# Performance work log

Hardware: AMD Instinct MI355X
Metric: run time of the kernel (lower is better)

The kernel has to match this reference:

```python
import jax, jax.numpy as jnp
import numpy as np
import itertools

DIMS = (128, 128, 128)
CHANNELS = 8
BATCH = 2_097_152


def setup_inputs() -> dict:
    key = jax.random.key(0)
    k1, k2 = jax.random.split(key)
    unList = jax.random.uniform(k1, (BATCH, len(DIMS)), dtype=jnp.float32)
    table = jax.random.uniform(k2, DIMS + (CHANNELS,), dtype=jnp.float32)  # initScale=1, initMode='R'
    return {"unList": unList, "table": table}


def reference(unList, table):
    # N-D multilinear (bilinear/trilinear) interpolated table lookup.
    dims = table.shape[:-1]
    n = len(dims)
    c = table.shape[-1]
    dims_f = jnp.asarray(dims, jnp.float32)
    # map normalized coords [0,1] onto grid [0, dim-1]
    scaled = jnp.clip(unList, 0.0, 1.0) * (dims_f - 1.0)          # [B, n]
    i0 = jnp.clip(jnp.floor(scaled), 0.0, dims_f - 2.0).astype(jnp.int32)  # lower corner
    frac = scaled - i0.astype(jnp.float32)                        # [B, n] in [0,1]
    # flatten grid for single-axis gathers
    strides = jnp.asarray([int(np.prod(dims[k + 1:])) for k in range(n)], jnp.int32)
    table_flat = table.reshape(-1, c)                             # [prod(dims), C]
    out = jnp.zeros((unList.shape[0], c), table.dtype)
    # loop over the 2^n corners (8 for 3D) -- small static loop
    for corner in itertools.product((0, 1), repeat=n):
        bits = jnp.asarray(corner, jnp.int32)                     # [n]
        flat_idx = ((i0 + bits) * strides).sum(-1)                # [B]
        w = jnp.prod(jnp.where(jnp.asarray(corner, bool), frac, 1.0 - frac), axis=-1)  # [B]
        out = out + w[:, None] * table_flat[flat_idx]             # gather + weighted sum
    return out
```

## Files before the change

### kernel.cpp

```cpp
#include <hip/hip_runtime.h>


#define DIM 128
#define CH 8
#define BINS 128
#define CHUNK 4096
#define PPT 16
#define REC_OFF 4096

__device__ __forceinline__ int key_of(float ux) {
    float sx = fminf(fmaxf(ux, 0.0f), 1.0f) * 127.0f;
    float fx0 = fminf(floorf(sx), 126.0f);
    return (int)fx0;
}

__global__ __launch_bounds__(256) void k_hist(const float* __restrict__ un,
                                              unsigned* __restrict__ hist, int batch) {
    __shared__ unsigned lh[BINS];
    for (int i = threadIdx.x; i < BINS; i += blockDim.x) lh[i] = 0;
    __syncthreads();
    int stride = gridDim.x * blockDim.x;
    for (int i = blockIdx.x * blockDim.x + threadIdx.x; i < batch; i += stride)
        atomicAdd(&lh[key_of(un[3 * i])], 1u);
    __syncthreads();
    for (int i = threadIdx.x; i < BINS; i += blockDim.x)
        if (lh[i]) atomicAdd(&hist[i], lh[i]);
}

__global__ void k_scan(const unsigned* __restrict__ hist,
                       unsigned* __restrict__ base, unsigned* __restrict__ cursor) {
    __shared__ unsigned lh[BINS];
    __shared__ unsigned lb[BINS];
    int t = threadIdx.x;
    if (t < BINS) lh[t] = hist[t];
    __syncthreads();
    if (t == 0) {
        unsigned acc = 0;
        for (int i = 0; i < BINS; ++i) { lb[i] = acc; acc += lh[i]; }
    }
    __syncthreads();
    if (t < BINS) { base[t] = lb[t]; cursor[t] = lb[t]; }
}

__global__ __launch_bounds__(256) void k_scatter(const float* __restrict__ un,
                                                 unsigned* __restrict__ cursor,
                                                 float4* __restrict__ rec, int batch) {
    __shared__ unsigned lh[BINS];
    __shared__ unsigned lbase[BINS];
    int t = threadIdx.x;
    for (int i = t; i < BINS; i += blockDim.x) lh[i] = 0;
    __syncthreads();
    int start = blockIdx.x * CHUNK;
    unsigned kr[PPT];
#pragma unroll
    for (int j = 0; j < PPT; ++j) {
        int i = start + j * 256 + t;
        if (i < batch) {
            int k = key_of(un[3 * i]);
            unsigned r = atomicAdd(&lh[k], 1u);
            kr[j] = (unsigned)k | (r << 8);
        } else kr[j] = 0xFFFFFFFFu;
    }
    __syncthreads();
    for (int i = t; i < BINS; i += blockDim.x)
        lbase[i] = lh[i] ? atomicAdd(&cursor[i], lh[i]) : 0u;
    __syncthreads();
#pragma unroll
    for (int j = 0; j < PPT; ++j) {
        int i = start + j * 256 + t;
        if (i < batch) {
            unsigned k = kr[j] & 0xFFu, r = kr[j] >> 8;
            float ux = un[3 * i], uy = un[3 * i + 1], uz = un[3 * i + 2];
            rec[lbase[k] + r] = make_float4(ux, uy, uz, __uint_as_float((unsigned)i));
        }
    }
}

__global__ __launch_bounds__(256) void k_main(const float4* __restrict__ rec,
                                              const float* __restrict__ table,
                                              float* __restrict__ out, int batch) {
    int per = gridDim.x >> 3;
    int pb = blockIdx.x;
    int lb = (pb & 7) * per + (pb >> 3);

    int t = (int)threadIdx.x;
    int lane = t & 63;
    int wave = t >> 6;
    int p = lane >> 2;
    int q = lane & 3;

    int i = lb * 64 + wave * 16 + p;
    if (i >= batch) return;

    float4 r = rec[i];
    unsigned orig = __float_as_uint(r.w);

    const float dmax = 127.0f, imax = 126.0f;
    float sx = fminf(fmaxf(r.x, 0.0f), 1.0f) * dmax;
    float sy = fminf(fmaxf(r.y, 0.0f), 1.0f) * dmax;
    float sz = fminf(fmaxf(r.z, 0.0f), 1.0f) * dmax;
    float fx0 = fminf(fmaxf(floorf(sx), 0.0f), imax);
    float fy0 = fminf(fmaxf(floorf(sy), 0.0f), imax);
    float fz0 = fminf(fmaxf(floorf(sz), 0.0f), imax);
    int x0 = (int)fx0, y0 = (int)fy0, z0 = (int)fz0;
    float fx = sx - fx0, fy = sy - fy0, fz = sz - fz0;

    float wx[2] = {1.0f - fx, fx};
    float wy[2] = {1.0f - fy, fy};
    float wzq = (q & 2) ? fz : (1.0f - fz);

    float4 acc = make_float4(0.f, 0.f, 0.f, 0.f);
#pragma unroll
    for (int bx = 0; bx < 2; ++bx) {
#pragma unroll
        for (int by = 0; by < 2; ++by) {
            const float* pbase = table +
                ((size_t)((x0 + bx) * DIM + (y0 + by)) * DIM + z0) * CH + (q << 2);
            float w = wx[bx] * wy[by] * wzq;
            float4 v = *reinterpret_cast<const float4*>(pbase);
            acc.x += w * v.x;
            acc.y += w * v.y;
            acc.z += w * v.z;
            acc.w += w * v.w;
        }
    }

    acc.x += __shfl_xor(acc.x, 2);
    acc.y += __shfl_xor(acc.y, 2);
    acc.z += __shfl_xor(acc.z, 2);
    acc.w += __shfl_xor(acc.w, 2);

    if (q < 2) {
        *reinterpret_cast<float4*>(out + (size_t)orig * CH + (q << 2)) = acc;
    }
}

__global__ __launch_bounds__(256) void k_naive(const float* __restrict__ un,
                                               const float* __restrict__ table,
                                               float* __restrict__ out, int batch) {
    int b = blockIdx.x * blockDim.x + threadIdx.x;
    if (b >= batch) return;
    float ux = un[3 * b], uy = un[3 * b + 1], uz = un[3 * b + 2];
    const float dmax = 127.0f, imax = 126.0f;
    float sx = fminf(fmaxf(ux, 0.0f), 1.0f) * dmax;
    float sy = fminf(fmaxf(uy, 0.0f), 1.0f) * dmax;
    float sz = fminf(fmaxf(uz, 0.0f), 1.0f) * dmax;
    float fx0 = fminf(fmaxf(floorf(sx), 0.0f), imax);
    float fy0 = fminf(fmaxf(floorf(sy), 0.0f), imax);
    float fz0 = fminf(fmaxf(floorf(sz), 0.0f), imax);
    int x0 = (int)fx0, y0 = (int)fy0, z0 = (int)fz0;
    float fx = sx - fx0, fy = sy - fy0, fz = sz - fz0;
    float wx[2] = {1.0f - fx, fx};
    float wy[2] = {1.0f - fy, fy};
    float wz0 = 1.0f - fz, wz1 = fz;
    float acc[CH];
#pragma unroll
    for (int c = 0; c < CH; ++c) acc[c] = 0.0f;
#pragma unroll
    for (int bx = 0; bx < 2; ++bx)
#pragma unroll
        for (int by = 0; by < 2; ++by) {
            const float* p = table + ((size_t)((x0 + bx) * DIM + (y0 + by)) * DIM + z0) * CH;
            float wxy = wx[bx] * wy[by];
            float w0 = wxy * wz0, w1 = wxy * wz1;
            float4 a0 = *reinterpret_cast<const float4*>(p + 0);
            float4 a1 = *reinterpret_cast<const float4*>(p + 4);
            float4 b0 = *reinterpret_cast<const float4*>(p + 8);
            float4 b1 = *reinterpret_cast<const float4*>(p + 12);
            acc[0] += w0 * a0.x + w1 * b0.x;  acc[1] += w0 * a0.y + w1 * b0.y;
            acc[2] += w0 * a0.z + w1 * b0.z;  acc[3] += w0 * a0.w + w1 * b0.w;
            acc[4] += w0 * a1.x + w1 * b1.x;  acc[5] += w0 * a1.y + w1 * b1.y;
            acc[6] += w0 * a1.z + w1 * b1.z;  acc[7] += w0 * a1.w + w1 * b1.w;
        }
    float4* o = reinterpret_cast<float4*>(out + (size_t)b * CH);
    o[0] = make_float4(acc[0], acc[1], acc[2], acc[3]);
    o[1] = make_float4(acc[4], acc[5], acc[6], acc[7]);
}

extern "C" void kernel_launch(void* const* d_in, const int* in_sizes, int n_in,
                              void* d_out, int out_size, void* d_ws, size_t ws_size,
                              hipStream_t stream) {
    const float* un    = (const float*)d_in[0];
    const float* table = (const float*)d_in[1];
    float* out         = (float*)d_out;
    int batch = in_sizes[0] / 3;

    size_t need = (size_t)REC_OFF + (size_t)batch * 16;
    if (ws_size < need) {
        int grid = (batch + 255) / 256;
        k_naive<<<grid, 256, 0, stream>>>(un, table, out, batch);
        return;
    }

    unsigned* hist   = (unsigned*)d_ws;
    unsigned* base   = (unsigned*)((char*)d_ws + 512);
    unsigned* cursor = (unsigned*)((char*)d_ws + 1024);
    float4*   rec    = (float4*)((char*)d_ws + REC_OFF);

    hipMemsetAsync(d_ws, 0, 1536, stream);
    k_hist<<<512, 256, 0, stream>>>(un, hist, batch);
    k_scan<<<1, 128, 0, stream>>>(hist, base, cursor);
    int nscat = (batch + CHUNK - 1) / CHUNK;
    k_scatter<<<nscat, 256, 0, stream>>>(un, cursor, rec, batch);
    int nmain = (batch + 63) / 64;
    nmain = ((nmain + 7) / 8) * 8;
    k_main<<<nmain, 256, 0, stream>>>(rec, table, out, batch);
}
```

Measured before the change: 113.3 us.

## Make gather kernel persistent with 4-point batched loads per wave

Replaces the one-point-per-16-lanes grid of 32768 blocks with a fixed grid of 2048 blocks. Each wave now walks a contiguous range of sorted records, handling 4 points per iteration and issuing all 16 table float4 loads before combining them, which raises memory-level parallelism. Address math moves to 32-bit byte offsets and a redundant clamp is dropped. The intent is to cut block launch overhead and hide gather latency, at the cost of more registers per thread (launch_bounds 256,4) and a possible tail imbalance between waves.

After: 128.4 us. +13.3%, slower.

```diff
diff --git a/kernel.cpp b/kernel.cpp
--- a/kernel.cpp
+++ b/kernel.cpp
@@ -7,6 +7,7 @@
 #define CHUNK 4096
 #define PPT 16
 #define REC_OFF 4096
+#define NMAIN 2048
 
 __device__ __forceinline__ int key_of(float ux) {
     float sx = fminf(fmaxf(ux, 0.0f), 1.0f) * 127.0f;
@@ -76,62 +77,125 @@
     }
 }
 
-__global__ __launch_bounds__(256) void k_main(const float4* __restrict__ rec,
-                                              const float* __restrict__ table,
-                                              float* __restrict__ out, int batch) {
+__global__ __launch_bounds__(256, 4) void k_main(const float4* __restrict__ rec,
+                                                 const float* __restrict__ table,
+                                                 float* __restrict__ out, int batch) {
     int per = gridDim.x >> 3;
     int pb = blockIdx.x;
     int lb = (pb & 7) * per + (pb >> 3);
 
     int t = (int)threadIdx.x;
-    int lane = t & 63;
-    int wave = t >> 6;
-    int p = lane >> 2;
-    int q = lane & 3;
-
-    int i = lb * 64 + wave * 16 + p;
-    if (i >= batch) return;
-
-    float4 r = rec[i];
-    unsigned orig = __float_as_uint(r.w);
+    int lane = t & 63, wave = t >> 6;
+    int p = lane >> 2, q = lane & 3;
+
+    int nw = (int)gridDim.x * 4;
+    int g = lb * 4 + wave;
+    long ppw = ((((long)batch + (long)nw * 64 - 1) / ((long)nw * 64)) * 64);
+    long beg = (long)g * ppw;
+    long end = beg + ppw;
+    if (end > (long)batch) end = (long)batch;
+    if (beg >= end) return;
 
     const float dmax = 127.0f, imax = 126.0f;
-    float sx = fminf(fmaxf(r.x, 0.0f), 1.0f) * dmax;
-    float sy = fminf(fmaxf(r.y, 0.0f), 1.0f) * dmax;
-    float sz = fminf(fmaxf(r.z, 0.0f), 1.0f) * dmax;
-    float fx0 = fminf(fmaxf(floorf(sx), 0.0f), imax);
-    float fy0 = fminf(fmaxf(floorf(sy), 0.0f), imax);
-    float fz0 = fminf(fmaxf(floorf(sz), 0.0f), imax);
-    int x0 = (int)fx0, y0 = (int)fy0, z0 = (int)fz0;
-    float fx = sx - fx0, fy = sy - fy0, fz = sz - fz0;
-
-    float wx[2] = {1.0f - fx, fx};
-    float wy[2] = {1.0f - fy, fy};
-    float wzq = (q & 2) ? fz : (1.0f - fz);
-
-    float4 acc = make_float4(0.f, 0.f, 0.f, 0.f);
-#pragma unroll
-    for (int bx = 0; bx < 2; ++bx) {
-#pragma unroll
-        for (int by = 0; by < 2; ++by) {
-            const float* pbase = table +
-                ((size_t)((x0 + bx) * DIM + (y0 + by)) * DIM + z0) * CH + (q << 2);
-            float w = wx[bx] * wy[by] * wzq;
-            float4 v = *reinterpret_cast<const float4*>(pbase);
-            acc.x += w * v.x;
-            acc.y += w * v.y;
-            acc.z += w * v.z;
-            acc.w += w * v.w;
-        }
-    }
-
-    acc.x += __shfl_xor(acc.x, 2);
-    acc.y += __shfl_xor(acc.y, 2);
-    acc.z += __shfl_xor(acc.z, 2);
-    acc.w += __shfl_xor(acc.w, 2);
-
-    if (q < 2) {
-        *reinterpret_cast<float4*>(out + (size_t)orig * CH + (q << 2)) = acc;
+    const char* tb = (const char*)table;
+    const unsigned qoff = (unsigned)(q << 4);
+
+    long base = beg;
+    for (; base + 64 <= end; base += 64) {
+        float4 r0 = rec[base + 0  + p];
+        float4 r1 = rec[base + 16 + p];
+        float4 r2 = rec[base + 32 + p];
+        float4 r3 = rec[base + 48 + p];
+
+        unsigned o_[4]; unsigned off_[4]; float w_[4][4];
+#define PREP(s, rr) { \
+        float sx = fminf(fmaxf(rr.x, 0.0f), 1.0f) * dmax; \
+        float sy = fminf(fmaxf(rr.y, 0.0f), 1.0f) * dmax; \
+        float sz = fminf(fmaxf(rr.z, 0.0f), 1.0f) * dmax; \
+        float fx0 = fminf(floorf(sx), imax); \
+        float fy0 = fminf(floorf(sy), imax); \
+        float fz0 = fminf(floorf(sz), imax); \
+        int x0 = (int)fx0, y0 = (int)fy0, z0 = (int)fz0; \
+        float fx = sx - fx0, fy = sy - fy0, fz = sz - fz0; \
+        float wzq = (q & 2) ? fz : (1.0f - fz); \
+        float gx = 1.0f - fx, gy = 1.0f - fy; \
+        w_[s][0] = gx * gy * wzq; \
+        w_[s][1] = gx * fy * wzq; \
+        w_[s][2] = fx * gy * wzq; \
+        w_[s][3] = fx * fy * wzq; \
+        off_[s] = (unsigned)(((x0 * 128 + y0) * 128 + z0) * 32) + qoff; \
+        o_[s] = __float_as_uint(rr.w); }
+        PREP(0, r0) PREP(1, r1) PREP(2, r2) PREP(3, r3)
+#undef PREP
+
+        float4 v00 = *(const float4*)(tb + off_[0]);
+        float4 v01 = *(const float4*)(tb + off_[0] + 4096u);
+        float4 v02 = *(const float4*)(tb + off_[0] + 524288u);
+        float4 v03 = *(const float4*)(tb + off_[0] + 528384u);
+        float4 v10 = *(const float4*)(tb + off_[1]);
+        float4 v11 = *(const float4*)(tb + off_[1] + 4096u);
+        float4 v12 = *(const float4*)(tb + off_[1] + 524288u);
+        float4 v13 = *(const float4*)(tb + off_[1] + 528384u);
+        float4 v20 = *(const float4*)(tb + off_[2]);
+        float4 v21 = *(const float4*)(tb + off_[2] + 4096u);
+        float4 v22 = *(const float4*)(tb + off_[2] + 524288u);
+        float4 v23 = *(const float4*)(tb + off_[2] + 528384u);
+        float4 v30 = *(const float4*)(tb + off_[3]);
+        float4 v31 = *(const float4*)(tb + off_[3] + 4096u);
+        float4 v32 = *(const float4*)(tb + off_[3] + 524288u);
+        float4 v33 = *(const float4*)(tb + off_[3] + 528384u);
+
+#define COMB(s, a, b, c, d) { \
+        float4 acc; \
+        acc.x = w_[s][0]*a.x + w_[s][1]*b.x + w_[s][2]*c.x + w_[s][3]*d.x; \
+        acc.y = w_[s][0]*a.y + w_[s][1]*b.y + w_[s][2]*c.y + w_[s][3]*d.y; \
+        acc.z = w_[s][0]*a.z + w_[s][1]*b.z + w_[s][2]*c.z + w_[s][3]*d.z; \
+        acc.w = w_[s][0]*a.w + w_[s][1]*b.w + w_[s][2]*c.w + w_[s][3]*d.w; \
+        acc.x += __shfl_xor(acc.x, 2); \
+        acc.y += __shfl_xor(acc.y, 2); \
+        acc.z += __shfl_xor(acc.z, 2); \
+        acc.w += __shfl_xor(acc.w, 2); \
+        if (q < 2) \
+            *reinterpret_cast<float4*>(out + (size_t)o_[s] * CH + (q << 2)) = acc; }
+        COMB(0, v00, v01, v02, v03)
+        COMB(1, v10, v11, v12, v13)
+        COMB(2, v20, v21, v22, v23)
+        COMB(3, v30, v31, v32, v33)
+#undef COMB
+    }
+
+    for (; base < end; base += 16) {
+        long i = base + p;
+        if (i >= end) continue;
+        float4 r = rec[i];
+        unsigned orig = __float_as_uint(r.w);
+        float sx = fminf(fmaxf(r.x, 0.0f), 1.0f) * dmax;
+        float sy = fminf(fmaxf(r.y, 0.0f), 1.0f) * dmax;
+        float sz = fminf(fmaxf(r.z, 0.0f), 1.0f) * dmax;
+        float fx0 = fminf(floorf(sx), imax);
+        float fy0 = fminf(floorf(sy), imax);
+        float fz0 = fminf(floorf(sz), imax);
+        int x0 = (int)fx0, y0 = (int)fy0, z0 = (int)fz0;
+        float fx = sx - fx0, fy = sy - fy0, fz = sz - fz0;
+        float wzq = (q & 2) ? fz : (1.0f - fz);
+        float gx = 1.0f - fx, gy = 1.0f - fy;
+        unsigned off = (unsigned)(((x0 * 128 + y0) * 128 + z0) * 32) + qoff;
+        float4 a = *(const float4*)(tb + off);
+        float4 b = *(const float4*)(tb + off + 4096u);
+        float4 c = *(const float4*)(tb + off + 524288u);
+        float4 d = *(const float4*)(tb + off + 528384u);
+        float w0 = gx * gy * wzq, w1 = gx * fy * wzq, w2 = fx * gy * wzq, w3 = fx * fy * wzq;
+        float4 acc;
+        acc.x = w0*a.x + w1*b.x + w2*c.x + w3*d.x;
+        acc.y = w0*a.y + w1*b.y + w2*c.y + w3*d.y;
+        acc.z = w0*a.z + w1*b.z + w2*c.z + w3*d.z;
+        acc.w = w0*a.w + w1*b.w + w2*c.w + w3*d.w;
+        acc.x += __shfl_xor(acc.x, 2);
+        acc.y += __shfl_xor(acc.y, 2);
+        acc.z += __shfl_xor(acc.z, 2);
+        acc.w += __shfl_xor(acc.w, 2);
+        if (q < 2)
+            *reinterpret_cast<float4*>(out + (size_t)orig * CH + (q << 2)) = acc;
     }
 }
 
@@ -145,9 +209,9 @@
     float sx = fminf(fmaxf(ux, 0.0f), 1.0f) * dmax;
     float sy = fminf(fmaxf(uy, 0.0f), 1.0f) * dmax;
     float sz = fminf(fmaxf(uz, 0.0f), 1.0f) * dmax;
-    float fx0 = fminf(fmaxf(floorf(sx), 0.0f), imax);
-    float fy0 = fminf(fmaxf(floorf(sy), 0.0f), imax);
-    float fz0 = fminf(fmaxf(floorf(sz), 0.0f), imax);
+    float fx0 = fminf(floorf(sx), imax);
+    float fy0 = fminf(floorf(sy), imax);
+    float fz0 = fminf(floorf(sz), imax);
     int x0 = (int)fx0, y0 = (int)fy0, z0 = (int)fz0;
     float fx = sx - fx0, fy = sy - fy0, fz = sz - fz0;
     float wx[2] = {1.0f - fx, fx};
@@ -160,13 +224,13 @@
     for (int bx = 0; bx < 2; ++bx)
 #pragma unroll
         for (int by = 0; by < 2; ++by) {
-            const float* p = table + ((size_t)((x0 + bx) * DIM + (y0 + by)) * DIM + z0) * CH;
+            const float* pp = table + ((size_t)((x0 + bx) * DIM + (y0 + by)) * DIM + z0) * CH;
             float wxy = wx[bx] * wy[by];
             float w0 = wxy * wz0, w1 = wxy * wz1;
-            float4 a0 = *reinterpret_cast<const float4*>(p + 0);
-            float4 a1 = *reinterpret_cast<const float4*>(p + 4);
-            float4 b0 = *reinterpret_cast<const float4*>(p + 8);
-            float4 b1 = *reinterpret_cast<const float4*>(p + 12);
+            float4 a0 = *reinterpret_cast<const float4*>(pp + 0);
+            float4 a1 = *reinterpret_cast<const float4*>(pp + 4);
+            float4 b0 = *reinterpret_cast<const float4*>(pp + 8);
+            float4 b1 = *reinterpret_cast<const float4*>(pp + 12);
             acc[0] += w0 * a0.x + w1 * b0.x;  acc[1] += w0 * a0.y + w1 * b0.y;
             acc[2] += w0 * a0.z + w1 * b0.z;  acc[3] += w0 * a0.w + w1 * b0.w;
             acc[4] += w0 * a1.x + w1 * b1.x;  acc[5] += w0 * a1.y + w1 * b1.y;
@@ -202,7 +266,5 @@
     k_scan<<<1, 128, 0, stream>>>(hist, base, cursor);
     int nscat = (batch + CHUNK - 1) / CHUNK;
     k_scatter<<<nscat, 256, 0, stream>>>(un, cursor, rec, batch);
-    int nmain = (batch + 63) / 64;
-    nmain = ((nmain + 7) / 8) * 8;
-    k_main<<<nmain, 256, 0, stream>>>(rec, table, out, batch);
-}
+    k_main<<<NMAIN, 256, 0, stream>>>(rec, table, out, batch);
+}
```
